# Optimization experiments

Measured on AMD Instinct MI355X. Metric: run time of the kernel, lower is better.

## Reference

```python
import jax, jax.numpy as jnp
import numpy as np

N_NODES = 100000
N_EDGES = 1600000
IN_FEAT = 64
OUT_FEAT = 64
NUM_RELS = 64
NUM_BASES = 2


def setup_inputs() -> dict:
    key = jax.random.key(0)
    ks = jax.random.split(key, 8)
    feat = jax.random.normal(ks[0], (N_NODES, IN_FEAT), dtype=jnp.float32)
    weight = jax.random.normal(ks[1], (NUM_BASES, IN_FEAT, OUT_FEAT), dtype=jnp.float32) * (1.0 / np.sqrt(IN_FEAT))
    w_comp = jax.random.normal(ks[2], (NUM_RELS, NUM_BASES), dtype=jnp.float32)
    loop_weight = jax.random.normal(ks[3], (IN_FEAT, OUT_FEAT), dtype=jnp.float32) * (1.0 / np.sqrt(IN_FEAT))
    h_bias = jnp.zeros((OUT_FEAT,), dtype=jnp.float32)
    src = jax.random.randint(ks[4], (N_EDGES,), 0, N_NODES, dtype=jnp.int32)
    dst = jax.random.randint(ks[5], (N_EDGES,), 0, N_NODES, dtype=jnp.int32)
    etypes = jax.random.randint(ks[6], (N_EDGES,), 0, NUM_RELS, dtype=jnp.int32)
    return {"feat": feat, "weight": weight, "w_comp": w_comp,
            "loop_weight": loop_weight, "h_bias": h_bias,
            "src": src, "dst": dst, "etypes": etypes}


def reference(feat, weight, w_comp, loop_weight, h_bias, src, dst, etypes):
    # Basis decomposition: W_r = sum_b w_comp[r, b] * V_b.
    # Instead of materializing per-edge (E, in, out) weights (the highmem
    # index_select), precompute the per-node, per-basis transform once
    # (N, B, out) and combine with the per-edge basis coefficients --
    # mathematically identical to msg_e = h[src_e] @ W_{etype_e}.
    hb = jnp.einsum('ni,bio->nbo', feat, weight)      # (N, B, out)
    coeff = w_comp[etypes]                             # (E, B)
    msg = jnp.einsum('ebo,eb->eo', hb[src], coeff)     # (E, out)
    # Sum aggregation into destination nodes (fn.sum('msg', 'h')).
    agg = jax.ops.segment_sum(msg, dst, num_segments=feat.shape[0])
    # Self-loop + bias (activation=None, dropout=0, layer_norm=False).
    return agg + feat @ loop_weight + h_bias
```

## Files before the change

kernel.cpp:

```cpp
#include <hip/hip_runtime.h>


constexpr int N_NODES  = 100000;
constexpr int N_EDGES  = 1600000;
constexpr int IN_FEAT  = 64;
constexpr int OUT_FEAT = 64;

constexpr int BN  = 256;
constexpr int NB  = (N_NODES + BN - 1) / BN;
constexpr int CAP = 4608;
constexpr int SC_CHUNK = 8192;

constexpr int NPG = 16;
constexpr int N_GRP = N_NODES / NPG;
constexpr int LROW = 200;

typedef __attribute__((ext_vector_type(8))) short bf16x8;
typedef __attribute__((ext_vector_type(4))) float f32x4;

__device__ __forceinline__ unsigned pack_entry(int d, int s, int r) {
    return (unsigned)(d & (BN - 1)) | ((unsigned)s << 8) | ((unsigned)r << 25);
}

__device__ __forceinline__ unsigned bf16_rne(float f) {
    unsigned b = __float_as_uint(f);
    b += 0x7fffu + ((b >> 16) & 1u);
    return b >> 16;
}

__global__ __launch_bounds__(256) void k_prep(const float* __restrict__ feat,
                                              unsigned* __restrict__ fbf,
                                              const float* __restrict__ weight,
                                              const float* __restrict__ loop_weight,
                                              unsigned short* __restrict__ wtb,
                                              int* __restrict__ bcursor) {
    const int b = blockIdx.x, t = threadIdx.x;
    if (b < 2048) {
        const int total = N_NODES * 16;
        const float4* __restrict__ f4 = (const float4*)feat;
        uint2* __restrict__ o2 = (uint2*)fbf;
        for (int i = b * 256 + t; i < total; i += 2048 * 256) {
            const float4 f = f4[i];
            uint2 o;
            o.x = bf16_rne(f.x) | (bf16_rne(f.y) << 16);
            o.y = bf16_rne(f.z) | (bf16_rne(f.w) << 16);
            o2[i] = o;
        }
    } else if (b < 2050) {
        const int i = (b - 2048) * 256 + t;
        if (i < NB) bcursor[i] = i * CAP;
    } else {
        const int idx = (b - 2050) * 256 + t;
        const int n = idx / LROW, r = idx % LROW;
        float v = 0.0f;
        if (r < 128)      v = weight[r * 64 + n];
        else if (r < 192) v = loop_weight[(r - 128) * 64 + n];
        wtb[idx] = (unsigned short)bf16_rne(v);
    }
}

__global__ __launch_bounds__(256) void k_bscatter(const int* __restrict__ src,
                                                  const int* __restrict__ dst,
                                                  const int* __restrict__ et,
                                                  int* __restrict__ bcursor,
                                                  unsigned* __restrict__ sorted_c) {
    __shared__ int hist[NB], gb[NB], lcur[NB];
    const int t = threadIdx.x;
    const int cbase = blockIdx.x * SC_CHUNK;
    for (int i = t; i < NB; i += 256) { hist[i] = 0; lcur[i] = 0; }
    __syncthreads();
    #pragma unroll 1
    for (int k = 0; k < SC_CHUNK / 256; ++k) {
        const int e = cbase + k * 256 + t;
        if (e < N_EDGES) atomicAdd(&hist[dst[e] >> 8], 1);
    }
    __syncthreads();
    for (int i = t; i < NB; i += 256) {
        const int c = hist[i];
        gb[i] = c ? atomicAdd(&bcursor[i], c) : 0;
    }
    __syncthreads();
    #pragma unroll 1
    for (int k = 0; k < SC_CHUNK / 256; ++k) {
        const int e = cbase + k * 256 + t;
        if (e < N_EDGES) {
            const int d = dst[e];
            const int bkt = d >> 8;
            const int r = atomicAdd(&lcur[bkt], 1);
            sorted_c[gb[bkt] + r] = pack_entry(d, src[e], et[e]);
        }
    }
}

__global__ __launch_bounds__(512) void k_fine(const unsigned* __restrict__ sorted_c,
                                              const int* __restrict__ bcursor,
                                              int* __restrict__ offs,
                                              int* __restrict__ ends,
                                              unsigned* __restrict__ sorted_f) {
    __shared__ int cnt[BN];
    __shared__ int part[BN];
    __shared__ int cur[BN];
    const int t = threadIdx.x;
    const int b = blockIdx.x;
    if (t < BN) cnt[t] = 0;
    __syncthreads();
    const int base = b * CAP;
    const int end  = bcursor[b];
    for (int k = base + t; k < end; k += 512)
        atomicAdd(&cnt[sorted_c[k] & (BN - 1)], 1);
    __syncthreads();
    int v = 0;
    if (t < BN) {
        v = cnt[t];
        part[t] = v;
    }
    __syncthreads();
    for (int d = 1; d < BN; d <<= 1) {
        const int u = (t < BN && t >= d) ? part[t - d] : 0;
        __syncthreads();
        if (t < BN) part[t] += u;
        __syncthreads();
    }
    if (t < BN) {
        const int node = b * BN + t;
        const int off = base + part[t] - v;
        if (node < N_NODES) { offs[node] = off; ends[node] = off + v; }
        cur[t] = off;
    }
    __syncthreads();
    for (int k = base + t; k < end; k += 512) {
        const unsigned en = sorted_c[k];
        const int pos = atomicAdd(&cur[en & (BN - 1)], 1);
        sorted_f[pos] = en;
    }
}

__global__ __launch_bounds__(512, 4) void k_gather_post(
    const int*      __restrict__ offs,
    const int*      __restrict__ ends,
    const unsigned* __restrict__ sorted_f,
    const float*    __restrict__ w_comp,
    const unsigned short* __restrict__ fbs,
    const unsigned short* __restrict__ wtb,
    const float*    __restrict__ h_bias,
    float*          __restrict__ out)
{
    __shared__ unsigned short WtS[64 * LROW];
    __shared__ unsigned short LinS[NPG * LROW];
    __shared__ float2 wcl[64];

    const int tid  = threadIdx.x;
    const int lane = tid & 63;
    const int w    = tid >> 6;

    {
        const unsigned* __restrict__ wsrc = (const unsigned*)wtb;
        unsigned* __restrict__ wdst = (unsigned*)WtS;
        for (int i = tid; i < 64 * LROW / 2; i += 512) wdst[i] = wsrc[i];
        if (tid < 64) wcl[tid] = ((const float2*)w_comp)[tid];
    }
    __syncthreads();

    const int grp = blockIdx.x;

    #pragma unroll 1
    for (int half = 0; half < 2; ++half) {
        const int slot = 2 * w + half;
        const int n = __builtin_amdgcn_readfirstlane(grp * NPG + slot);
        const int start = __builtin_amdgcn_readfirstlane(offs[n]);
        const int end   = __builtin_amdgcn_readfirstlane(ends[n]);

        float a0 = 0.f, b0 = 0.f, a1 = 0.f, b1 = 0.f;
        int k = start;
        for (; k + 7 < end; k += 8) {
            unsigned p[8]; float f[8];
            #pragma unroll
            for (int i = 0; i < 8; ++i) p[i] = sorted_f[k + i];
            #pragma unroll
            for (int i = 0; i < 8; ++i)
                f[i] = __uint_as_float(
                    (unsigned)fbs[(size_t)((p[i] >> 8) & 0x1FFFF) * 64 + lane] << 16);
            #pragma unroll
            for (int i = 0; i < 8; ++i) {
                const float2 c = wcl[p[i] >> 25];
                if (i & 1) { a1 = fmaf(c.x, f[i], a1); b1 = fmaf(c.y, f[i], b1); }
                else       { a0 = fmaf(c.x, f[i], a0); b0 = fmaf(c.y, f[i], b0); }
            }
        }
        for (; k + 3 < end; k += 4) {
            unsigned p[4]; float f[4];
            #pragma unroll
            for (int i = 0; i < 4; ++i) p[i] = sorted_f[k + i];
            #pragma unroll
            for (int i = 0; i < 4; ++i)
                f[i] = __uint_as_float(
                    (unsigned)fbs[(size_t)((p[i] >> 8) & 0x1FFFF) * 64 + lane] << 16);
            #pragma unroll
            for (int i = 0; i < 4; ++i) {
                const float2 c = wcl[p[i] >> 25];
                if (i & 1) { a1 = fmaf(c.x, f[i], a1); b1 = fmaf(c.y, f[i], b1); }
                else       { a0 = fmaf(c.x, f[i], a0); b0 = fmaf(c.y, f[i], b0); }
            }
        }
        for (; k < end; ++k) {
            const unsigned p0 = sorted_f[k];
            const float f0 = __uint_as_float(
                (unsigned)fbs[(size_t)((p0 >> 8) & 0x1FFFF) * 64 + lane] << 16);
            const float2 c0 = wcl[p0 >> 25];
            a0 = fmaf(c0.x, f0, a0); b0 = fmaf(c0.y, f0, b0);
        }
        LinS[slot * LROW + lane]       = (unsigned short)bf16_rne(a0 + a1);
        LinS[slot * LROW + 64 + lane]  = (unsigned short)bf16_rne(b0 + b1);
        LinS[slot * LROW + 128 + lane] = fbs[(size_t)n * 64 + lane];
    }
    __syncthreads();

    if (w < 4) {
        const int r16 = lane & 15;
        const int q   = lane >> 4;
        const float bv = h_bias[w * 16 + r16];
        f32x4 acc = {bv, bv, bv, bv};
        #pragma unroll
        for (int kt = 0; kt < 6; ++kt) {
            const bf16x8 a = *(const bf16x8*)&LinS[r16 * LROW + kt * 32 + q * 8];
            const bf16x8 b = *(const bf16x8*)&WtS[(w * 16 + r16) * LROW + kt * 32 + q * 8];
            acc = __builtin_amdgcn_mfma_f32_16x16x32_bf16(a, b, acc, 0, 0, 0);
        }
        #pragma unroll
        for (int r = 0; r < 4; ++r)
            out[(size_t)(grp * NPG + q * 4 + r) * 64 + w * 16 + r16] = acc[r];
    }
}

extern "C" void kernel_launch(void* const* d_in, const int* in_sizes, int n_in,
                              void* d_out, int out_size, void* d_ws, size_t ws_size,
                              hipStream_t stream) {
    const float* feat        = (const float*)d_in[0];
    const float* weight      = (const float*)d_in[1];
    const float* w_comp      = (const float*)d_in[2];
    const float* loop_weight = (const float*)d_in[3];
    const float* h_bias      = (const float*)d_in[4];
    const int*   src         = (const int*)d_in[5];
    const int*   dst         = (const int*)d_in[6];
    const int*   etypes      = (const int*)d_in[7];
    float* out = (float*)d_out;

    unsigned* sorted_c = (unsigned*)d_ws;
    unsigned* sorted_f = sorted_c + (size_t)NB * CAP;
    unsigned* fbf      = sorted_f + (size_t)NB * CAP;
    unsigned* wtbu     = fbf + N_NODES * 32;
    int*      offs     = (int*)(wtbu + 64 * LROW / 2);
    int*      ends     = offs + N_NODES;
    int*      bcursor  = ends + N_NODES;

    k_prep<<<2100, 256, 0, stream>>>(feat, fbf, weight, loop_weight,
                                     (unsigned short*)wtbu, bcursor);
    k_bscatter<<<(N_EDGES + SC_CHUNK - 1) / SC_CHUNK, 256, 0, stream>>>(
        src, dst, etypes, bcursor, sorted_c);
    k_fine<<<NB, 512, 0, stream>>>(sorted_c, bcursor, offs, ends, sorted_f);
    k_gather_post<<<N_GRP, 512, 0, stream>>>(offs, ends, sorted_f, w_comp,
                                             (const unsigned short*)fbf,
                                             (const unsigned short*)wtbu,
                                             h_bias, out);
}
```

Measured before the change: 124.2 us.

## Fuse edge bucket scatter with feature conversion and interleave two-node gathers

```diff
diff --git a/kernel.cpp b/kernel.cpp
--- a/kernel.cpp
+++ b/kernel.cpp
@@ -10,6 +10,9 @@
 constexpr int NB  = (N_NODES + BN - 1) / BN;
 constexpr int CAP = 4608;
 constexpr int SC_CHUNK = 8192;
+constexpr int NCH = (N_EDGES + SC_CHUNK - 1) / SC_CHUNK;
+constexpr int CVT_BLOCKS = 1024;
+constexpr int W_BLOCKS = 50;
 
 constexpr int NPG = 16;
 constexpr int N_GRP = N_NODES / NPG;
@@ -28,29 +31,56 @@
     return b >> 16;
 }
 
-__global__ __launch_bounds__(256) void k_prep(const float* __restrict__ feat,
-                                              unsigned* __restrict__ fbf,
-                                              const float* __restrict__ weight,
-                                              const float* __restrict__ loop_weight,
-                                              unsigned short* __restrict__ wtb,
-                                              int* __restrict__ bcursor) {
+__global__ __launch_bounds__(256) void k_scatter_prep(
+    const int* __restrict__ src, const int* __restrict__ dst,
+    const int* __restrict__ et,  int* __restrict__ bcnt,
+    unsigned* __restrict__ sorted_c,
+    const float* __restrict__ feat, unsigned* __restrict__ fbf,
+    const float* __restrict__ weight, const float* __restrict__ loop_weight,
+    unsigned short* __restrict__ wtb)
+{
+    __shared__ int hist[NB], gb[NB], lcur[NB];
     const int b = blockIdx.x, t = threadIdx.x;
-    if (b < 2048) {
+
+    if (b < NCH) {
+        const int cbase = b * SC_CHUNK;
+        for (int i = t; i < NB; i += 256) { hist[i] = 0; lcur[i] = 0; }
+        __syncthreads();
+        #pragma unroll 1
+        for (int k = 0; k < SC_CHUNK / 256; ++k) {
+            const int e = cbase + k * 256 + t;
+            if (e < N_EDGES) atomicAdd(&hist[dst[e] >> 8], 1);
+        }
+        __syncthreads();
+        for (int i = t; i < NB; i += 256) {
+            const int c = hist[i];
+            gb[i] = c ? (i * CAP + atomicAdd(&bcnt[i], c)) : 0;
+        }
+        __syncthreads();
+        #pragma unroll 1
+        for (int k = 0; k < SC_CHUNK / 256; ++k) {
+            const int e = cbase + k * 256 + t;
+            if (e < N_EDGES) {
+                const int d = dst[e];
+                const int bkt = d >> 8;
+                const int r = atomicAdd(&lcur[bkt], 1);
+                sorted_c[gb[bkt] + r] = pack_entry(d, src[e], et[e]);
+            }
+        }
+    } else if (b < NCH + CVT_BLOCKS) {
+        const int bb = b - NCH;
         const int total = N_NODES * 16;
         const float4* __restrict__ f4 = (const float4*)feat;
         uint2* __restrict__ o2 = (uint2*)fbf;
-        for (int i = b * 256 + t; i < total; i += 2048 * 256) {
+        for (int i = bb * 256 + t; i < total; i += CVT_BLOCKS * 256) {
             const float4 f = f4[i];
             uint2 o;
             o.x = bf16_rne(f.x) | (bf16_rne(f.y) << 16);
             o.y = bf16_rne(f.z) | (bf16_rne(f.w) << 16);
             o2[i] = o;
         }
-    } else if (b < 2050) {
-        const int i = (b - 2048) * 256 + t;
-        if (i < NB) bcursor[i] = i * CAP;
     } else {
-        const int idx = (b - 2050) * 256 + t;
+        const int idx = (b - NCH - CVT_BLOCKS) * 256 + t;
         const int n = idx / LROW, r = idx % LROW;
         float v = 0.0f;
         if (r < 128)      v = weight[r * 64 + n];
@@ -59,41 +89,8 @@
     }
 }
 
-__global__ __launch_bounds__(256) void k_bscatter(const int* __restrict__ src,
-                                                  const int* __restrict__ dst,
-                                                  const int* __restrict__ et,
-                                                  int* __restrict__ bcursor,
-                                                  unsigned* __restrict__ sorted_c) {
-    __shared__ int hist[NB], gb[NB], lcur[NB];
-    const int t = threadIdx.x;
-    const int cbase = blockIdx.x * SC_CHUNK;
-    for (int i = t; i < NB; i += 256) { hist[i] = 0; lcur[i] = 0; }
-    __syncthreads();
-    #pragma unroll 1
-    for (int k = 0; k < SC_CHUNK / 256; ++k) {
-        const int e = cbase + k * 256 + t;
-        if (e < N_EDGES) atomicAdd(&hist[dst[e] >> 8], 1);
-    }
-    __syncthreads();
-    for (int i = t; i < NB; i += 256) {
-        const int c = hist[i];
-        gb[i] = c ? atomicAdd(&bcursor[i], c) : 0;
-    }
-    __syncthreads();
-    #pragma unroll 1
-    for (int k = 0; k < SC_CHUNK / 256; ++k) {
-        const int e = cbase + k * 256 + t;
-        if (e < N_EDGES) {
-            const int d = dst[e];
-            const int bkt = d >> 8;
-            const int r = atomicAdd(&lcur[bkt], 1);
-            sorted_c[gb[bkt] + r] = pack_entry(d, src[e], et[e]);
-        }
-    }
-}
-
 __global__ __launch_bounds__(512) void k_fine(const unsigned* __restrict__ sorted_c,
-                                              const int* __restrict__ bcursor,
+                                              const int* __restrict__ bcnt,
                                               int* __restrict__ offs,
                                               int* __restrict__ ends,
                                               unsigned* __restrict__ sorted_f) {
@@ -105,7 +102,7 @@
     if (t < BN) cnt[t] = 0;
     __syncthreads();
     const int base = b * CAP;
-    const int end  = bcursor[b];
+    const int end  = base + bcnt[b];
     for (int k = base + t; k < end; k += 512)
         atomicAdd(&cnt[sorted_c[k] & (BN - 1)], 1);
     __syncthreads();
@@ -163,19 +160,51 @@
 
     const int grp = blockIdx.x;
 
-    #pragma unroll 1
-    for (int half = 0; half < 2; ++half) {
-        const int slot = 2 * w + half;
-        const int n = __builtin_amdgcn_readfirstlane(grp * NPG + slot);
-        const int start = __builtin_amdgcn_readfirstlane(offs[n]);
-        const int end   = __builtin_amdgcn_readfirstlane(ends[n]);
-
-        float a0 = 0.f, b0 = 0.f, a1 = 0.f, b1 = 0.f;
-        int k = start;
-        for (; k + 7 < end; k += 8) {
+    {
+        const int nA = __builtin_amdgcn_readfirstlane(grp * NPG + 2 * w);
+        const int nB = nA + 1;
+        const int sA = __builtin_amdgcn_readfirstlane(offs[nA]);
+        const int eA = __builtin_amdgcn_readfirstlane(ends[nA]);
+        const int sB = __builtin_amdgcn_readfirstlane(offs[nB]);
+        const int eB = __builtin_amdgcn_readfirstlane(ends[nB]);
+
+        float aA0 = 0.f, bA0 = 0.f, aA1 = 0.f, bA1 = 0.f;
+        float aB0 = 0.f, bB0 = 0.f, aB1 = 0.f, bB1 = 0.f;
+        int kA = sA, kB = sB;
+
+        while (kA + 7 < eA && kB + 7 < eB) {
+            unsigned pA[8], pB[8]; float fA[8], fB[8];
+            #pragma unroll
+            for (int i = 0; i < 8; ++i) pA[i] = sorted_f[kA + i];
+            #pragma unroll
+            for (int i = 0; i < 8; ++i) pB[i] = sorted_f[kB + i];
+            #pragma unroll
+            for (int i = 0; i < 8; ++i)
+                fA[i] = __uint_as_float(
+                    (unsigned)fbs[(size_t)((pA[i] >> 8) & 0x1FFFF) * 64 + lane] << 16);
+            #pragma unroll
+            for (int i = 0; i < 8; ++i)
+                fB[i] = __uint_as_float(
+                    (unsigned)fbs[(size_t)((pB[i] >> 8) & 0x1FFFF) * 64 + lane] << 16);
+            #pragma unroll
+            for (int i = 0; i < 8; ++i) {
+                const float2 c = wcl[pA[i] >> 25];
+                if (i & 1) { aA1 = fmaf(c.x, fA[i], aA1); bA1 = fmaf(c.y, fA[i], bA1); }
+                else       { aA0 = fmaf(c.x, fA[i], aA0); bA0 = fmaf(c.y, fA[i], bA0); }
+            }
+            #pragma unroll
+            for (int i = 0; i < 8; ++i) {
+                const float2 c = wcl[pB[i] >> 25];
+                if (i & 1) { aB1 = fmaf(c.x, fB[i], aB1); bB1 = fmaf(c.y, fB[i], bB1); }
+                else       { aB0 = fmaf(c.x, fB[i], aB0); bB0 = fmaf(c.y, fB[i], bB0); }
+            }
+            kA += 8; kB += 8;
+        }
+
+        for (; kA + 7 < eA; kA += 8) {
             unsigned p[8]; float f[8];
             #pragma unroll
-            for (int i = 0; i < 8; ++i) p[i] = sorted_f[k + i];
+            for (int i = 0; i < 8; ++i) p[i] = sorted_f[kA + i];
             #pragma unroll
             for (int i = 0; i < 8; ++i)
                 f[i] = __uint_as_float(
@@ -183,14 +212,14 @@
             #pragma unroll
             for (int i = 0; i < 8; ++i) {
                 const float2 c = wcl[p[i] >> 25];
-                if (i & 1) { a1 = fmaf(c.x, f[i], a1); b1 = fmaf(c.y, f[i], b1); }
-                else       { a0 = fmaf(c.x, f[i], a0); b0 = fmaf(c.y, f[i], b0); }
-            }
-        }
-        for (; k + 3 < end; k += 4) {
+                if (i & 1) { aA1 = fmaf(c.x, f[i], aA1); bA1 = fmaf(c.y, f[i], bA1); }
+                else       { aA0 = fmaf(c.x, f[i], aA0); bA0 = fmaf(c.y, f[i], bA0); }
+            }
+        }
+        for (; kA + 3 < eA; kA += 4) {
             unsigned p[4]; float f[4];
             #pragma unroll
-            for (int i = 0; i < 4; ++i) p[i] = sorted_f[k + i];
+            for (int i = 0; i < 4; ++i) p[i] = sorted_f[kA + i];
             #pragma unroll
             for (int i = 0; i < 4; ++i)
                 f[i] = __uint_as_float(
@@ -198,20 +227,63 @@
             #pragma unroll
             for (int i = 0; i < 4; ++i) {
                 const float2 c = wcl[p[i] >> 25];
-                if (i & 1) { a1 = fmaf(c.x, f[i], a1); b1 = fmaf(c.y, f[i], b1); }
-                else       { a0 = fmaf(c.x, f[i], a0); b0 = fmaf(c.y, f[i], b0); }
-            }
-        }
-        for (; k < end; ++k) {
-            const unsigned p0 = sorted_f[k];
+                if (i & 1) { aA1 = fmaf(c.x, f[i], aA1); bA1 = fmaf(c.y, f[i], bA1); }
+                else       { aA0 = fmaf(c.x, f[i], aA0); bA0 = fmaf(c.y, f[i], bA0); }
+            }
+        }
+        for (; kA < eA; ++kA) {
+            const unsigned p0 = sorted_f[kA];
             const float f0 = __uint_as_float(
                 (unsigned)fbs[(size_t)((p0 >> 8) & 0x1FFFF) * 64 + lane] << 16);
             const float2 c0 = wcl[p0 >> 25];
-            a0 = fmaf(c0.x, f0, a0); b0 = fmaf(c0.y, f0, b0);
-        }
-        LinS[slot * LROW + lane]       = (unsigned short)bf16_rne(a0 + a1);
-        LinS[slot * LROW + 64 + lane]  = (unsigned short)bf16_rne(b0 + b1);
-        LinS[slot * LROW + 128 + lane] = fbs[(size_t)n * 64 + lane];
+            aA0 = fmaf(c0.x, f0, aA0); bA0 = fmaf(c0.y, f0, bA0);
+        }
+
+        for (; kB + 7 < eB; kB += 8) {
+            unsigned p[8]; float f[8];
+            #pragma unroll
+            for (int i = 0; i < 8; ++i) p[i] = sorted_f[kB + i];
+            #pragma unroll
+            for (int i = 0; i < 8; ++i)
+                f[i] = __uint_as_float(
+                    (unsigned)fbs[(size_t)((p[i] >> 8) & 0x1FFFF) * 64 + lane] << 16);
+            #pragma unroll
+            for (int i = 0; i < 8; ++i) {
+                const float2 c = wcl[p[i] >> 25];
+                if (i & 1) { aB1 = fmaf(c.x, f[i], aB1); bB1 = fmaf(c.y, f[i], bB1); }
+                else       { aB0 = fmaf(c.x, f[i], aB0); bB0 = fmaf(c.y, f[i], bB0); }
+            }
+        }
+        for (; kB + 3 < eB; kB += 4) {
+            unsigned p[4]; float f[4];
+            #pragma unroll
+            for (int i = 0; i < 4; ++i) p[i] = sorted_f[kB + i];
+            #pragma unroll
+            for (int i = 0; i < 4; ++i)
+                f[i] = __uint_as_float(
+                    (unsigned)fbs[(size_t)((p[i] >> 8) & 0x1FFFF) * 64 + lane] << 16);
+            #pragma unroll
+            for (int i = 0; i < 4; ++i) {
+                const float2 c = wcl[p[i] >> 25];
+                if (i & 1) { aB1 = fmaf(c.x, f[i], aB1); bB1 = fmaf(c.y, f[i], bB1); }
+                else       { aB0 = fmaf(c.x, f[i], aB0); bB0 = fmaf(c.y, f[i], bB0); }
+            }
+        }
+        for (; kB < eB; ++kB) {
+            const unsigned p0 = sorted_f[kB];
+            const float f0 = __uint_as_float(
+                (unsigned)fbs[(size_t)((p0 >> 8) & 0x1FFFF) * 64 + lane] << 16);
+            const float2 c0 = wcl[p0 >> 25];
+            aB0 = fmaf(c0.x, f0, aB0); bB0 = fmaf(c0.y, f0, bB0);
+        }
+
+        const int slotA = 2 * w, slotB = 2 * w + 1;
+        LinS[slotA * LROW + lane]       = (unsigned short)bf16_rne(aA0 + aA1);
+        LinS[slotA * LROW + 64 + lane]  = (unsigned short)bf16_rne(bA0 + bA1);
+        LinS[slotA * LROW + 128 + lane] = fbs[(size_t)nA * 64 + lane];
+        LinS[slotB * LROW + lane]       = (unsigned short)bf16_rne(aB0 + aB1);
+        LinS[slotB * LROW + 64 + lane]  = (unsigned short)bf16_rne(bB0 + bB1);
+        LinS[slotB * LROW + 128 + lane] = fbs[(size_t)nB * 64 + lane];
     }
     __syncthreads();
 
@@ -251,13 +323,13 @@
     unsigned* wtbu     = fbf + N_NODES * 32;
     int*      offs     = (int*)(wtbu + 64 * LROW / 2);
     int*      ends     = offs + N_NODES;
-    int*      bcursor  = ends + N_NODES;
-
-    k_prep<<<2100, 256, 0, stream>>>(feat, fbf, weight, loop_weight,
-                                     (unsigned short*)wtbu, bcursor);
-    k_bscatter<<<(N_EDGES + SC_CHUNK - 1) / SC_CHUNK, 256, 0, stream>>>(
-        src, dst, etypes, bcursor, sorted_c);
-    k_fine<<<NB, 512, 0, stream>>>(sorted_c, bcursor, offs, ends, sorted_f);
+    int*      bcnt     = ends + N_NODES;
+
+    hipMemsetAsync(bcnt, 0, NB * sizeof(int), stream);
+    k_scatter_prep<<<NCH + CVT_BLOCKS + W_BLOCKS, 256, 0, stream>>>(
+        src, dst, etypes, bcnt, sorted_c, feat, fbf, weight, loop_weight,
+        (unsigned short*)wtbu);
+    k_fine<<<NB, 512, 0, stream>>>(sorted_c, bcnt, offs, ends, sorted_f);
     k_gather_post<<<N_GRP, 512, 0, stream>>>(offs, ends, sorted_f, w_comp,
                                              (const unsigned short*)fbf,
                                              (const unsigned short*)wtbu,
```

New measurement: 121.8 us. About the same (-1.9%).
